# Optimization experiments

Hardware: AMD Instinct MI355X
Metric: run time of the kernel (lower is better)

The kernel has to match this reference:

```python
import math
import jax, jax.numpy as jnp
from jax import lax
import numpy as np

SQRT2 = 1.4142135623730951
LR_MLP = 0.01


def _blur_kernel():
    k = jnp.array([1., 3., 3., 1.], dtype=jnp.float32)
    k = k[:, None] * k[None, :]
    return k / jnp.sum(k)


def upfirdn2d(x, kernel, up, pad0, pad1):
    # x: (B,C,H,W). Matches torch upfirdn2d_native (flip kernel, zero-upsample, pad, correlate).
    B, C, H, W = x.shape
    x = x.reshape(B * C, 1, H, W)
    k = jnp.flip(kernel, (0, 1))[None, None]
    p1 = pad1 + (up - 1)  # lax lhs_dilation omits trailing zeros of upfirdn upsampling
    out = lax.conv_general_dilated(x, k, (1, 1), ((pad0, p1), (pad0, p1)), lhs_dilation=(up, up))
    return out.reshape(B, C, out.shape[-2], out.shape[-1])


def pixel_norm(x, eps=1e-6):
    norm = jnp.sqrt(jnp.sum(x * x, axis=1, keepdims=True))
    norm = norm / math.sqrt(x.shape[1])
    return x / (norm + eps)


def fused_act(x, b):
    return jax.nn.leaky_relu(x + b[None, :, None, None], 0.2) * SQRT2


def mod_conv(x, w, sw, sb, lat, demodulate, up):
    # w: (Cout,Cin,kh,kw); sw: (Cin, style_ch) equalized-lr linear; lat: (B, style_ch)
    Cout, Cin, kh, kw = w.shape
    s = lat @ (sw.T * (1.0 / math.sqrt(sw.shape[1]))) + sb  # (B, Cin), bias_init=1
    wm = (w * (1.0 / math.sqrt(Cin * kh * kw)))[None] * s[:, None, :, None, None]
    if demodulate:
        d = lax.rsqrt(jnp.sum(wm * wm, axis=(2, 3, 4)) + 1e-8)
        wm = wm * d[:, :, None, None, None]
    if up:
        # per-sample conv_transpose(stride=2, pad=0) == dilated conv with flipped kernel
        def f(xi, wi):
            return lax.conv_general_dilated(xi[None], jnp.flip(wi, (2, 3)), (1, 1),
                                            ((kh - 1, kh - 1), (kw - 1, kw - 1)),
                                            lhs_dilation=(2, 2))[0]
        out = jax.vmap(f)(x, wm)
        out = upfirdn2d(out, _blur_kernel() * 4.0, 1, 1, 1)  # Blur pad=(1,1), k*factor^2
    else:
        pad = kh // 2
        def f(xi, wi):
            return lax.conv_general_dilated(xi[None], wi, (1, 1), ((pad, pad), (pad, pad)))[0]
        out = jax.vmap(f)(x, wm)
    return out


def style_mapping(z, W, Bv):
    x = pixel_norm(z)
    sc = 1.0 / math.sqrt(W.shape[-1])
    for i in range(W.shape[0]):
        x = jax.nn.leaky_relu(x @ (W[i].T * sc) + Bv[i] * LR_MLP, 0.2) * SQRT2
    return x


def setup_inputs() -> dict:
    key = jax.random.key(0)
    ks = jax.random.split(key, 32)
    B = 32
    inp = {
        'z': jax.random.normal(ks[0], (B, 512), jnp.float32),
        'mlp_w': jax.random.normal(ks[1], (8, 512, 512), jnp.float32),
        'mlp_b': jax.random.normal(ks[2], (8, 512), jnp.float32),
        'const_input': jax.random.normal(ks[3], (1, 512, 4, 4), jnp.float32),
        'conv_w': jax.random.normal(ks[4], (9, 512, 512, 3, 3), jnp.float32),
        'conv_style_w': jax.random.normal(ks[5], (9, 512, 512), jnp.float32),
        'conv_style_b': jnp.ones((9, 512), jnp.float32),
        'noise_w': jax.random.normal(ks[6], (9,), jnp.float32),
        'act_bias': jnp.zeros((9, 512), jnp.float32),
        'torgb_w': jax.random.normal(ks[7], (5, 3, 512, 1, 1), jnp.float32),
        'torgb_style_w': jax.random.normal(ks[8], (5, 512, 512), jnp.float32),
        'torgb_style_b': jnp.ones((5, 512), jnp.float32),
        'torgb_bias': jnp.zeros((5, 3), jnp.float32),
    }
    sizes = [4, 8, 8, 16, 16, 32, 32, 64, 64]
    for i, s in enumerate(sizes):
        inp[f'noise{i}'] = jax.random.normal(ks[10 + i], (B, 1, s, s), jnp.float32)
    return inp


def reference(z, mlp_w, mlp_b, const_input, conv_w, conv_style_w, conv_style_b,
              noise_w, act_bias, torgb_w, torgb_style_w, torgb_style_b, torgb_bias,
              noise0, noise1, noise2, noise3, noise4, noise5, noise6, noise7, noise8):
    noises = [noise0, noise1, noise2, noise3, noise4, noise5, noise6, noise7, noise8]
    w = style_mapping(z, mlp_w, mlp_b)  # single style injection -> same w for all layers
    B = z.shape[0]
    x = jnp.tile(const_input, (B, 1, 1, 1))

    def sconv(x, i, up):
        out = mod_conv(x, conv_w[i], conv_style_w[i], conv_style_b[i], w, True, up)
        out = out + noise_w[i] * noises[i]
        return fused_act(out, act_bias[i])

    def trgb(x, j):
        out = mod_conv(x, torgb_w[j], torgb_style_w[j], torgb_style_b[j], w, False, False)
        return out + torgb_bias[j][None, :, None, None]

    x = sconv(x, 0, False)
    skip = trgb(x, 0)
    bk = _blur_kernel() * 4.0
    for r in range(4):  # resolutions 8,16,32,64
        x = sconv(x, 1 + 2 * r, True)
        x = sconv(x, 2 + 2 * r, False)
        skip = trgb(x, r + 1) + upfirdn2d(skip, bk, 2, 2, 1)  # UpsampleUpFIRDn pad=(2,1)
    return skip  # (B,3,64,64)
```

## Files before the change

kernel.cpp:

```cpp
#include <hip/hip_runtime.h>
#include <hip/hip_bf16.h>
#include <cstdio>
#include <math.h>


static constexpr int NB = 32;
static constexpr float SQRT2F      = 1.41421356237309515f;
static constexpr float INV_SQRT512 = 0.04419417382415922f;
static constexpr float INV_SQRT4608= 0.014731391274719742f;

typedef __hip_bfloat16 bf16;
typedef __attribute__((ext_vector_type(8))) short bf16x8;
typedef __attribute__((ext_vector_type(4))) float f32x4;

__device__ __forceinline__ float lrelu_s2(float v){ return (v > 0.f ? v : 0.2f*v) * SQRT2F; }
__device__ __forceinline__ float bf_lo(unsigned u){ unsigned v = u << 16; return __builtin_bit_cast(float, v); }
__device__ __forceinline__ float bf_hi(unsigned u){ unsigned v = u & 0xffff0000u; return __builtin_bit_cast(float, v); }
__device__ __forceinline__ unsigned packbf2(float a, float b){
  bf16 ha = __float2bfloat16(a), hb = __float2bfloat16(b);
  unsigned short ra = __builtin_bit_cast(unsigned short, ha);
  unsigned short rb = __builtin_bit_cast(unsigned short, hb);
  return (unsigned)ra | ((unsigned)rb << 16);
}

__global__ void k_mapping(const float* __restrict__ z, const float* __restrict__ mlp_w,
                          const float* __restrict__ mlp_b, float* __restrict__ wlat){
  __shared__ float xb[512], yb[512], red[256];
  int b = blockIdx.x, t = threadIdx.x;
  float z0 = z[b*512 + t], z1 = z[b*512 + t + 256];
  red[t] = z0*z0 + z1*z1;
  __syncthreads();
  for(int s = 128; s > 0; s >>= 1){ if(t < s) red[t] += red[t+s]; __syncthreads(); }
  float norm = sqrtf(red[0]) * INV_SQRT512;
  float inv = 1.f / (norm + 1e-6f);
  xb[t] = z0*inv; xb[t+256] = z1*inv;
  __syncthreads();
  for(int l = 0; l < 8; l++){
    const float* Wl = mlp_w + (size_t)l*512*512;
    const float* bl = mlp_b + l*512;
    for(int oo = 0; oo < 2; oo++){
      int o = t + oo*256;
      const float4* wr = (const float4*)(Wl + (size_t)o*512);
      float acc = 0.f;
      #pragma unroll 4
      for(int k = 0; k < 128; k++){
        float4 w4 = wr[k];
        acc += w4.x*xb[4*k] + w4.y*xb[4*k+1] + w4.z*xb[4*k+2] + w4.w*xb[4*k+3];
      }
      yb[o] = lrelu_s2(acc*INV_SQRT512 + bl[o]*0.01f);
    }
    __syncthreads();
    xb[t] = yb[t]; xb[t+256] = yb[t+256];
    __syncthreads();
  }
  wlat[b*512+t] = xb[t]; wlat[b*512+t+256] = xb[t+256];
}

__global__ void k_styles(const float* __restrict__ wlat,
                         const float* __restrict__ csw, const float* __restrict__ csb,
                         const float* __restrict__ tsw, const float* __restrict__ tsb,
                         float* __restrict__ s_conv, float* __restrict__ s_trgb){
  int gid = blockIdx.x*256 + threadIdx.x;
  int l = gid >> 14;
  int b = (gid >> 9) & 31;
  int i = gid & 511;
  const float* row; float bias, wsc;
  if(l < 9){ row = csw + ((size_t)l*512 + i)*512; bias = csb[l*512+i]; wsc = INV_SQRT4608; }
  else     { int lt = l-9; row = tsw + ((size_t)lt*512 + i)*512; bias = tsb[lt*512+i]; wsc = INV_SQRT512; }
  const float4* r4 = (const float4*)row;
  const float4* w4 = (const float4*)(wlat + b*512);
  float acc = 0.f;
  #pragma unroll 4
  for(int k = 0; k < 128; k++){
    float4 a = w4[k], c = r4[k];
    acc += a.x*c.x + a.y*c.y + a.z*c.z + a.w*c.w;
  }
  float s = (acc*INV_SQRT512 + bias) * wsc;
  if(l < 9) s_conv[((size_t)l*32 + b)*512 + i] = s;
  else      s_trgb[((size_t)(l-9)*32 + b)*512 + i] = s;
}

__global__ void k_wsq(const float* __restrict__ cw, float* __restrict__ wsq){
  int gid = blockIdx.x*256 + threadIdx.x;
  const float* p = cw + (size_t)gid*9;
  float a = 0.f;
  #pragma unroll
  for(int t = 0; t < 9; t++){ float v = p[t]; a += v*v; }
  wsq[gid] = a;
}

__global__ void k_demod(const float* __restrict__ s_conv, const float* __restrict__ wsq,
                        float* __restrict__ d_conv){
  __shared__ float s2[512];
  int l = blockIdx.x/32, b = blockIdx.x%32, t = threadIdx.x;
  size_t base = ((size_t)l*32 + b)*512;
  float v0 = s_conv[base + t], v1 = s_conv[base + t + 256];
  s2[t] = v0*v0; s2[t+256] = v1*v1;
  __syncthreads();
  for(int oo = 0; oo < 2; oo++){
    int o = t + oo*256;
    const float4* wr = (const float4*)(wsq + ((size_t)l*512 + o)*512);
    float acc = 0.f;
    #pragma unroll 4
    for(int k = 0; k < 128; k++){
      float4 w = wr[k];
      acc += w.x*s2[4*k] + w.y*s2[4*k+1] + w.z*s2[4*k+2] + w.w*s2[4*k+3];
    }
    d_conv[base + o] = rsqrtf(acc + 1e-8f);
  }
}

__global__ void k_ratio(const float* __restrict__ s_conv, const float* __restrict__ s_trgb,
                        float* __restrict__ rat){
  int gid = blockIdx.x*256 + threadIdx.x;
  int lt = gid >> 14;
  if(lt >= 4){ rat[gid] = 1.0f; return; }
  int b = (gid >> 9) & 31;
  int i = gid & 511;
  int cl = 1 + 2*lt;
  float st = s_trgb[((size_t)lt*32 + b)*512 + i];
  float sc = s_conv[((size_t)cl*32 + b)*512 + i];
  rat[gid] = (sc != 0.f) ? st/sc : 0.f;
}

__global__ void k_wB(const float* __restrict__ cw, bf16* __restrict__ wB){
  int gid = blockIdx.x*256 + threadIdx.x;
  const float* p = cw + (size_t)gid*9;
  int l = gid >> 18;
  int oi = gid & 0x3ffff;
  #pragma unroll
  for(int tap = 0; tap < 9; tap++)
    wB[((size_t)(l*9 + tap) << 18) + oi] = __float2bfloat16(p[tap]);
}

__global__ void k_init(const float* __restrict__ ci, const float* __restrict__ s_conv,
                       bf16* __restrict__ act){
  int gid = blockIdx.x*256 + threadIdx.x;
  int c = gid & 511; int px = (gid >> 9) & 15; int b = gid >> 13;
  act[gid] = __float2bfloat16(ci[c*16 + px] * s_conv[b*512 + c]);
}

template<bool UP>
__global__ __launch_bounds__(256, 2)
void k_conv(const bf16* __restrict__ act, const bf16* __restrict__ wL,
            const float* __restrict__ dL, const float* __restrict__ noise,
            const float* __restrict__ nw_ptr, const float* __restrict__ ab,
            const float* __restrict__ sN, bf16* __restrict__ outp,
            int Hin, int Mblocks){
  const int q8 = gridDim.x >> 3;
  const int swz = (blockIdx.x & 7)*q8 + (blockIdx.x >> 3);
  const int nb = swz & 3, mb = swz >> 2;
  if(mb >= Mblocks) return;
  const int mbase = mb*128, nbase = nb*128;

  int py = 0, px = 0;
  int OHy, OHx;
  if(UP){
    int cls = blockIdx.z; py = cls >> 1; px = cls & 1;
    OHy = Hin + 1 - py; OHx = Hin + 1 - px;
  } else {
    OHy = Hin; OHx = Hin;
  }
  const int pixN = OHy*OHx;
  const int Mtot = NB*pixN;
  if(mbase >= Mtot) return;

  __shared__ short As[2][128*40];
  __shared__ short Bs[2][128*40];
  const int t = threadIdx.x;
  const int slot = t & 3;
  const int rowq[2] = {t >> 2, (t >> 2) + 64};

  int gb[2], gY[2], gX[2]; bool mval[2];
  #pragma unroll
  for(int q = 0; q < 2; q++){
    int m = mbase + rowq[q];
    mval[q] = (m < Mtot);
    int mm = mval[q] ? m : 0;
    gb[q] = mm / pixN; int rem = mm % pixN; gY[q] = rem / OHx; gX[q] = rem % OHx;
  }

  const int wid = t >> 6;
  const int mrow0 = (wid >> 1)*64;
  const int ncol0 = (wid & 1)*64;
  const int lr = t & 15;
  const int ks = (t & 63) >> 4;

  f32x4 acc[4][4];
  #pragma unroll
  for(int i = 0; i < 4; i++)
    #pragma unroll
    for(int j = 0; j < 4; j++) acc[i][j] = (f32x4){0.f,0.f,0.f,0.f};

  int dyl[3], dxl[3], ndy, ndx;
  if(UP){
    if(py == 0){ dyl[0]=0; dyl[1]=2; ndy=2; } else { dyl[0]=1; ndy=1; }
    if(px == 0){ dxl[0]=0; dxl[1]=2; ndx=2; } else { dxl[0]=1; ndx=1; }
  } else {
    dyl[0]=0; dyl[1]=1; dyl[2]=2; ndy=3;
    dxl[0]=0; dxl[1]=1; dxl[2]=2; ndx=3;
  }
  const int TT = ndy*ndx;

  for(int tt = 0; tt < TT; tt++){
    const int dy = dyl[tt/ndx], dx = dxl[tt%ndx];
    const int tap = dy*3 + dx;
    const bf16* aptr[2]; bool aok[2];
    #pragma unroll
    for(int q = 0; q < 2; q++){
      aok[q] = false; aptr[q] = act;
      if(mval[q]){
        int yy, xx;
        if(UP){ yy = gY[q] - ((dy - py) >> 1); xx = gX[q] - ((dx - px) >> 1); }
        else  { yy = gY[q] + dy - 1;           xx = gX[q] + dx - 1; }
        if((unsigned)yy < (unsigned)Hin && (unsigned)xx < (unsigned)Hin){
          aok[q] = true;
          aptr[q] = act + ((size_t)((gb[q]*Hin + yy)*Hin + xx) << 9) + slot*8;
        }
      }
    }
    const bf16* bptr[2];
    #pragma unroll
    for(int q = 0; q < 2; q++)
      bptr[q] = wL + (((size_t)tap*512 + nbase + rowq[q]) << 9) + slot*8;

    uint4 pa[2][2], pb[2][2];
    #pragma unroll
    for(int q = 0; q < 2; q++)
      #pragma unroll
      for(int h = 0; h < 2; h++){
        pa[q][h] = aok[q] ? *(const uint4*)(aptr[q] + h*32) : make_uint4(0u,0u,0u,0u);
        pb[q][h] = *(const uint4*)(bptr[q] + h*32);
      }

    #pragma unroll
    for(int c = 0; c < 8; c++){
      asm volatile("" ::: "memory");
      __builtin_amdgcn_s_barrier();
      #pragma unroll
      for(int q = 0; q < 2; q++)
        #pragma unroll
        for(int h = 0; h < 2; h++){
          *(uint4*)&As[h][rowq[q]*40 + slot*8] = pa[q][h];
          *(uint4*)&Bs[h][rowq[q]*40 + slot*8] = pb[q][h];
        }
      uint4 na[2][2], nb4[2][2];
      if(c < 7){
        const int koff = (c+1)*64;
        #pragma unroll
        for(int q = 0; q < 2; q++)
          #pragma unroll
          for(int h = 0; h < 2; h++){
            na[q][h]  = aok[q] ? *(const uint4*)(aptr[q] + koff + h*32) : make_uint4(0u,0u,0u,0u);
            nb4[q][h] = *(const uint4*)(bptr[q] + koff + h*32);
          }
      }
      asm volatile("s_waitcnt lgkmcnt(0)" ::: "memory");
      __builtin_amdgcn_s_barrier();
      #pragma unroll
      for(int h = 0; h < 2; h++){
        bf16x8 af[4], bfr[4];
        #pragma unroll
        for(int f = 0; f < 4; f++){
          af[f]  = *(const bf16x8*)&As[h][(mrow0 + f*16 + lr)*40 + ks*8];
          bfr[f] = *(const bf16x8*)&Bs[h][(ncol0 + f*16 + lr)*40 + ks*8];
        }
        #pragma unroll
        for(int mf = 0; mf < 4; mf++)
          #pragma unroll
          for(int nf = 0; nf < 4; nf++)
            acc[mf][nf] = __builtin_amdgcn_mfma_f32_16x16x32_bf16(af[mf], bfr[nf], acc[mf][nf], 0, 0, 0);
      }
      if(c < 7){
        #pragma unroll
        for(int q = 0; q < 2; q++)
          #pragma unroll
          for(int h = 0; h < 2; h++){ pa[q][h] = na[q][h]; pb[q][h] = nb4[q][h]; }
      }
    }
  }

  const float nwv = UP ? 0.f : *nw_ptr;
  const int U = 2*Hin + 1;
  #pragma unroll
  for(int mf = 0; mf < 4; mf++){
    #pragma unroll
    for(int r = 0; r < 4; r++){
      int m = mbase + mrow0 + mf*16 + ks*4 + r;
      if(m >= Mtot) continue;
      int b = m / pixN; int rem = m % pixN; int y = rem / OHx, x = rem % OHx;
      const float* drow = dL + b*512;
      bf16* orow;
      float nz = 0.f; const float* srow = nullptr;
      if(UP){
        orow = outp + (((size_t)((b*U + 2*y + py))*U + (2*x + px)) << 9);
      } else {
        nz = nwv * noise[(b*OHy + y)*OHx + x];
        srow = sN + b*512;
        orow = outp + ((size_t)m << 9);
      }
      #pragma unroll
      for(int nf = 0; nf < 4; nf++){
        int n = nbase + ncol0 + nf*16 + lr;
        float val = acc[mf][nf][r] * drow[n];
        if(!UP) val = lrelu_s2(val + nz + ab[n]) * srow[n];
        orow[n] = __float2bfloat16(val);
      }
    }
  }
}

__global__ void k_blur(const bf16* __restrict__ u, const float* __restrict__ noise,
                       const float* __restrict__ nw_ptr, const float* __restrict__ ab,
                       const float* __restrict__ sN, bf16* __restrict__ act, int O){
  const int U = O + 1;
  size_t gid = (size_t)blockIdx.x*256 + threadIdx.x;
  size_t total = (size_t)NB*O*O*128;
  if(gid >= total) return;
  int c4 = gid & 127;
  size_t pix = gid >> 7;
  int X = pix % O; int Y = (pix/O) % O; int b = pix/((size_t)O*O);
  const float k1[4] = {1.f, 3.f, 3.f, 1.f};
  float4 a = make_float4(0.f,0.f,0.f,0.f);
  #pragma unroll
  for(int ky = 0; ky < 4; ky++){
    int yy = Y + ky - 1; if(yy < 0 || yy >= U) continue;
    #pragma unroll
    for(int kx = 0; kx < 4; kx++){
      int xx = X + kx - 1; if(xx < 0 || xx >= U) continue;
      float w = k1[ky]*k1[kx]*(1.f/16.f);
      uint2 u2 = *(const uint2*)(u + (((size_t)(b*U + yy)*U + xx) << 9) + c4*4);
      a.x += w*bf_lo(u2.x); a.y += w*bf_hi(u2.x);
      a.z += w*bf_lo(u2.y); a.w += w*bf_hi(u2.y);
    }
  }
  float nz = (*nw_ptr) * noise[(b*O + Y)*O + X];
  const float* abp4 = ab + c4*4;
  float4 s4 = *(const float4*)(sN + b*512 + c4*4);
  uint2 pk;
  pk.x = packbf2(lrelu_s2(a.x + nz + abp4[0])*s4.x, lrelu_s2(a.y + nz + abp4[1])*s4.y);
  pk.y = packbf2(lrelu_s2(a.z + nz + abp4[2])*s4.z, lrelu_s2(a.w + nz + abp4[3])*s4.w);
  *(uint2*)(act + (pix << 9) + c4*4) = pk;
}

__global__ void k_torgb(const bf16* __restrict__ act, const float* __restrict__ tw,
                        const float* __restrict__ ratL, const float* __restrict__ tbias,
                        float* __restrict__ dst, int H, int lt, int addflag){
  int wid = threadIdx.x >> 6, lane = threadIdx.x & 63;
  int pix = blockIdx.x*4 + wid;
  int npix = NB*H*H;
  if(pix >= npix) return;
  int b = pix/(H*H);
  const bf16* ap = act + ((size_t)pix << 9);
  const float* rp = ratL + (size_t)b*512;
  const float* w0 = tw + ((size_t)lt*3 + 0)*512;
  const float* w1 = tw + ((size_t)lt*3 + 1)*512;
  const float* w2 = tw + ((size_t)lt*3 + 2)*512;
  float a0 = 0.f, a1 = 0.f, a2 = 0.f;
  #pragma unroll
  for(int j = 0; j < 8; j++){
    int i = lane + j*64;
    float xs = __bfloat162float(ap[i])*rp[i];
    a0 += xs*w0[i]; a1 += xs*w1[i]; a2 += xs*w2[i];
  }
  for(int off = 32; off > 0; off >>= 1){
    a0 += __shfl_xor(a0, off);
    a1 += __shfl_xor(a1, off);
    a2 += __shfl_xor(a2, off);
  }
  if(lane == 0){
    int rem = pix % (H*H);
    size_t o0 = ((size_t)(b*3 + 0)*H*H) + rem;
    size_t o1 = ((size_t)(b*3 + 1)*H*H) + rem;
    size_t o2 = ((size_t)(b*3 + 2)*H*H) + rem;
    float b0 = tbias[lt*3+0], b1 = tbias[lt*3+1], b2 = tbias[lt*3+2];
    if(addflag){ dst[o0] += a0 + b0; dst[o1] += a1 + b1; dst[o2] += a2 + b2; }
    else       { dst[o0]  = a0 + b0; dst[o1]  = a1 + b1; dst[o2]  = a2 + b2; }
  }
}

__global__ void k_skipup(const float* __restrict__ sin, float* __restrict__ sout, int h){
  const int O = 2*h;
  int gid = blockIdx.x*256 + threadIdx.x;
  int total = NB*3*O*O;
  if(gid >= total) return;
  int X = gid % O; int Y = (gid/O) % O; int c = (gid/(O*O)) % 3; int b = gid/(3*O*O);
  const float k1[4] = {1.f, 3.f, 3.f, 1.f};
  float acc = 0.f;
  for(int ky = (Y & 1); ky < 4; ky += 2){
    int ty = Y + ky - 2;
    if(ty < 0) continue;
    int y = ty >> 1; if(y >= h) continue;
    for(int kx = (X & 1); kx < 4; kx += 2){
      int tx = X + kx - 2;
      if(tx < 0) continue;
      int x = tx >> 1; if(x >= h) continue;
      acc += k1[ky]*k1[kx]*(1.f/16.f) * sin[((size_t)(b*3 + c)*h + y)*h + x];
    }
  }
  sout[gid] = acc;
}

extern "C" void kernel_launch(void* const* d_in, const int* in_sizes, int n_in,
                              void* d_out, int out_size, void* d_ws, size_t ws_size,
                              hipStream_t stream){
  const float* z     = (const float*)d_in[0];
  const float* mlp_w = (const float*)d_in[1];
  const float* mlp_b = (const float*)d_in[2];
  const float* cinp  = (const float*)d_in[3];
  const float* conv_w= (const float*)d_in[4];
  const float* csw   = (const float*)d_in[5];
  const float* csb   = (const float*)d_in[6];
  const float* nwp   = (const float*)d_in[7];
  const float* abp   = (const float*)d_in[8];
  const float* tw    = (const float*)d_in[9];
  const float* tsw   = (const float*)d_in[10];
  const float* tsb   = (const float*)d_in[11];
  const float* tb    = (const float*)d_in[12];
  const float* noise[9];
  for(int i = 0; i < 9; i++) noise[i] = (const float*)d_in[13 + i];

  const size_t UMAX = (size_t)32*65*65*512;
  char* base = (char*)d_ws;
  size_t off = 0;
  bf16* buf0 = (bf16*)(base + off); off += UMAX*2;
  bf16* buf1 = (bf16*)(base + off); off += UMAX*2;
  bf16* wB   = (bf16*)(base + off); off += (size_t)9*9*512*512*2;
  float* wsq = (float*)(base + off); off += (size_t)9*512*512*4;
  float* wlat= (float*)(base + off); off += (size_t)32*512*4;
  float* sconv=(float*)(base + off); off += (size_t)9*32*512*4;
  float* dconv=(float*)(base + off); off += (size_t)9*32*512*4;
  float* strgb=(float*)(base + off); off += (size_t)5*32*512*4;
  float* rat  =(float*)(base + off); off += (size_t)5*32*512*4;
  float* skipA=(float*)(base + off); off += (size_t)32*3*64*64*4;
  float* skipB=(float*)(base + off); off += (size_t)32*3*64*64*4;
  if(ws_size < off){
    fprintf(stderr, "kernel_launch: ws too small (%zu < %zu)\n", ws_size, off);
    return;
  }
  float* out = (float*)d_out;

  k_mapping<<<32, 256, 0, stream>>>(z, mlp_w, mlp_b, wlat);
  k_styles <<<896, 256, 0, stream>>>(wlat, csw, csb, tsw, tsb, sconv, strgb);
  k_wsq    <<<9216, 256, 0, stream>>>(conv_w, wsq);
  k_demod  <<<288, 256, 0, stream>>>(sconv, wsq, dconv);
  k_ratio  <<<320, 256, 0, stream>>>(sconv, strgb, rat);
  k_wB     <<<9216, 256, 0, stream>>>(conv_w, wB);
  k_init   <<<1024, 256, 0, stream>>>(cinp, sconv, buf0);

  auto conv_noup = [&](const bf16* in, bf16* o, int H, int layer, const float* sN){
    int M = 32*H*H; int Mb = (M + 127)/128;
    int Gx = ((Mb*4 + 7)/8)*8;
    k_conv<false><<<dim3(Gx,1,1), 256, 0, stream>>>(in, wB + ((size_t)layer*9 << 18),
        dconv + (size_t)layer*NB*512, noise[layer], nwp + layer, abp + layer*512, sN, o, H, Mb);
  };
  auto conv_up = [&](const bf16* in, bf16* o, int Hin, int layer){
    int Mmax = 32*(Hin+1)*(Hin+1); int Mb = (Mmax + 127)/128;
    int Gx = ((Mb*4 + 7)/8)*8;
    k_conv<true><<<dim3(Gx,1,4), 256, 0, stream>>>(in, wB + ((size_t)layer*9 << 18),
        dconv + (size_t)layer*NB*512, nullptr, nullptr, nullptr, nullptr, o, Hin, Mb);
  };
  auto blur = [&](const bf16* u, bf16* o, int O, int layer, const float* sN){
    size_t total = (size_t)32*O*O*128;
    k_blur<<<(unsigned)((total + 255)/256), 256, 0, stream>>>(u, noise[layer], nwp + layer,
        abp + layer*512, sN, o, O);
  };
  auto torgb = [&](const bf16* act, float* dst, int H, int lt, int add){
    int npix = 32*H*H;
    k_torgb<<<(npix + 3)/4, 256, 0, stream>>>(act, tw, rat + (size_t)lt*NB*512, tb, dst, H, lt, add);
  };
  auto skipup = [&](const float* sin, float* sout, int h){
    int total = 32*3*(2*h)*(2*h);
    k_skipup<<<(total + 255)/256, 256, 0, stream>>>(sin, sout, h);
  };

  const float* S = sconv;
  const float* sT4 = strgb + (size_t)4*NB*512;

  conv_noup(buf0, buf1, 4, 0, S + (size_t)1*NB*512);
  torgb(buf1, skipA, 4, 0, 0);

  conv_up(buf1, buf0, 4, 1);
  blur(buf0, buf1, 8, 1, S + (size_t)2*NB*512);
  conv_noup(buf1, buf0, 8, 2, S + (size_t)3*NB*512);
  skipup(skipA, skipB, 4);
  torgb(buf0, skipB, 8, 1, 1);

  conv_up(buf0, buf1, 8, 3);
  blur(buf1, buf0, 16, 3, S + (size_t)4*NB*512);
  conv_noup(buf0, buf1, 16, 4, S + (size_t)5*NB*512);
  skipup(skipB, skipA, 8);
  torgb(buf1, skipA, 16, 2, 1);

  conv_up(buf1, buf0, 16, 5);
  blur(buf0, buf1, 32, 5, S + (size_t)6*NB*512);
  conv_noup(buf1, buf0, 32, 6, S + (size_t)7*NB*512);
  skipup(skipA, skipB, 16);
  torgb(buf0, skipB, 32, 3, 1);

  conv_up(buf0, buf1, 32, 7);
  blur(buf1, buf0, 64, 7, S + (size_t)8*NB*512);
  conv_noup(buf0, buf1, 64, 8, sT4);
  skipup(skipB, out, 32);
  torgb(buf1, out, 64, 4, 1);
}
```

Measured before the change: 2.528 ms.

## Fuse weight prep kernels and flatten conv tap/K loop into single pipelined loop

Merges the weight-squared and bf16 weight-transpose kernels into one pass over conv weights, so the fp32 weights are read once instead of twice. In the conv kernel, the per-tap outer loop plus unrolled 8-chunk inner loop become a single flattened loop over tap×chunk. The next tap's first chunk is now prefetched during the current tap's last compute, which removes the pipeline bubble at each tap boundary. Each thread now loads one row with two 16-element halves instead of two rows, which changes the global load pattern and adds per-iteration tap-setup logic.

```diff
diff --git a/kernel.cpp b/kernel.cpp
--- a/kernel.cpp
+++ b/kernel.cpp
@@ -80,13 +80,19 @@
   else      s_trgb[((size_t)(l-9)*32 + b)*512 + i] = s;
 }
 
-__global__ void k_wsq(const float* __restrict__ cw, float* __restrict__ wsq){
+__global__ void k_prep(const float* __restrict__ cw, float* __restrict__ wsq,
+                       bf16* __restrict__ wB){
   int gid = blockIdx.x*256 + threadIdx.x;
   const float* p = cw + (size_t)gid*9;
-  float a = 0.f;
-  #pragma unroll
-  for(int t = 0; t < 9; t++){ float v = p[t]; a += v*v; }
+  int l = gid >> 18;
+  int oi = gid & 0x3ffff;
+  float v[9]; float a = 0.f;
+  #pragma unroll
+  for(int t = 0; t < 9; t++){ v[t] = p[t]; a += v[t]*v[t]; }
   wsq[gid] = a;
+  #pragma unroll
+  for(int tap = 0; tap < 9; tap++)
+    wB[((size_t)(l*9 + tap) << 18) + oi] = __float2bfloat16(v[tap]);
 }
 
 __global__ void k_demod(const float* __restrict__ s_conv, const float* __restrict__ wsq,
@@ -123,16 +129,6 @@
   rat[gid] = (sc != 0.f) ? st/sc : 0.f;
 }
 
-__global__ void k_wB(const float* __restrict__ cw, bf16* __restrict__ wB){
-  int gid = blockIdx.x*256 + threadIdx.x;
-  const float* p = cw + (size_t)gid*9;
-  int l = gid >> 18;
-  int oi = gid & 0x3ffff;
-  #pragma unroll
-  for(int tap = 0; tap < 9; tap++)
-    wB[((size_t)(l*9 + tap) << 18) + oi] = __float2bfloat16(p[tap]);
-}
-
 __global__ void k_init(const float* __restrict__ ci, const float* __restrict__ s_conv,
                        bf16* __restrict__ act){
   int gid = blockIdx.x*256 + threadIdx.x;
@@ -168,17 +164,14 @@
   __shared__ short As[2][128*40];
   __shared__ short Bs[2][128*40];
   const int t = threadIdx.x;
-  const int slot = t & 3;
-  const int rowq[2] = {t >> 2, (t >> 2) + 64};
-
-  int gb[2], gY[2], gX[2]; bool mval[2];
-  #pragma unroll
-  for(int q = 0; q < 2; q++){
-    int m = mbase + rowq[q];
-    mval[q] = (m < Mtot);
-    int mm = mval[q] ? m : 0;
-    gb[q] = mm / pixN; int rem = mm % pixN; gY[q] = rem / OHx; gX[q] = rem % OHx;
-  }
+  const int row = t & 127;
+  const int sp  = (t >> 7) & 1;
+
+  int m = mbase + row;
+  const bool mval = (m < Mtot);
+  int mm = mval ? m : 0;
+  const int gb = mm / pixN; int rem = mm % pixN;
+  const int gY = rem / OHx, gX = rem % OHx;
 
   const int wid = t >> 6;
   const int mrow0 = (wid >> 1)*64;
@@ -192,91 +185,84 @@
     #pragma unroll
     for(int j = 0; j < 4; j++) acc[i][j] = (f32x4){0.f,0.f,0.f,0.f};
 
-  int dyl[3], dxl[3], ndy, ndx;
-  if(UP){
-    if(py == 0){ dyl[0]=0; dyl[1]=2; ndy=2; } else { dyl[0]=1; ndy=1; }
-    if(px == 0){ dxl[0]=0; dxl[1]=2; ndx=2; } else { dxl[0]=1; ndx=1; }
-  } else {
-    dyl[0]=0; dyl[1]=1; dyl[2]=2; ndy=3;
-    dxl[0]=0; dxl[1]=1; dxl[2]=2; ndx=3;
-  }
+  int ndy, ndx;
+  if(UP){ ndy = (py==0)?2:1; ndx = (px==0)?2:1; } else { ndy = 3; ndx = 3; }
   const int TT = ndy*ndx;
-
-  for(int tt = 0; tt < TT; tt++){
-    const int dy = dyl[tt/ndx], dx = dxl[tt%ndx];
-    const int tap = dy*3 + dx;
-    const bf16* aptr[2]; bool aok[2];
-    #pragma unroll
-    for(int q = 0; q < 2; q++){
-      aok[q] = false; aptr[q] = act;
-      if(mval[q]){
-        int yy, xx;
-        if(UP){ yy = gY[q] - ((dy - py) >> 1); xx = gX[q] - ((dx - px) >> 1); }
-        else  { yy = gY[q] + dy - 1;           xx = gX[q] + dx - 1; }
-        if((unsigned)yy < (unsigned)Hin && (unsigned)xx < (unsigned)Hin){
-          aok[q] = true;
-          aptr[q] = act + ((size_t)((gb[q]*Hin + yy)*Hin + xx) << 9) + slot*8;
+  const int TOT = TT*8;
+
+  const bf16* browB = wL + (((size_t)(nbase + row)) << 9) + sp*16;
+
+  const bf16* aptr = act; const bf16* bptr = browB; bool aok = false;
+  auto setTap = [&](int tt){
+    int iy, ix;
+    if(!UP){ iy = (tt*11) >> 5; ix = tt - iy*3; }
+    else   { iy = (ndx==2) ? (tt>>1) : tt; ix = tt & (ndx-1); }
+    int dy = UP ? ((py==0) ? iy*2 : 1) : iy;
+    int dx = UP ? ((px==0) ? ix*2 : 1) : ix;
+    int yy, xx;
+    if(UP){ yy = gY - ((dy - py) >> 1); xx = gX - ((dx - px) >> 1); }
+    else  { yy = gY + dy - 1;           xx = gX + dx - 1; }
+    aok = mval && ((unsigned)yy < (unsigned)Hin) && ((unsigned)xx < (unsigned)Hin);
+    aptr = act + ((size_t)((gb*Hin + yy)*Hin + xx) << 9) + sp*16;
+    bptr = browB + ((size_t)(dy*3 + dx) << 18);
+  };
+
+  setTap(0);
+  uint4 pa[2][2], pb[2][2];
+  #pragma unroll
+  for(int h = 0; h < 2; h++)
+    #pragma unroll
+    for(int j = 0; j < 2; j++){
+      pa[h][j] = aok ? *(const uint4*)(aptr + h*32 + j*8) : make_uint4(0u,0u,0u,0u);
+      pb[h][j] = *(const uint4*)(bptr + h*32 + j*8);
+    }
+
+  for(int it = 0; it < TOT; ++it){
+    asm volatile("" ::: "memory");
+    __builtin_amdgcn_s_barrier();
+    #pragma unroll
+    for(int h = 0; h < 2; h++)
+      #pragma unroll
+      for(int j = 0; j < 2; j++){
+        *(uint4*)&As[h][row*40 + sp*16 + j*8] = pa[h][j];
+        *(uint4*)&Bs[h][row*40 + sp*16 + j*8] = pb[h][j];
+      }
+    uint4 na[2][2], nb4[2][2];
+    const bool have = (it + 1 < TOT);
+    if(have){
+      const int itn = it + 1;
+      const int cn = itn & 7;
+      if(cn == 0) setTap(itn >> 3);
+      const int icc = cn*64;
+      #pragma unroll
+      for(int h = 0; h < 2; h++)
+        #pragma unroll
+        for(int j = 0; j < 2; j++){
+          na[h][j]  = aok ? *(const uint4*)(aptr + icc + h*32 + j*8) : make_uint4(0u,0u,0u,0u);
+          nb4[h][j] = *(const uint4*)(bptr + icc + h*32 + j*8);
         }
+    }
+    asm volatile("s_waitcnt lgkmcnt(0)" ::: "memory");
+    __builtin_amdgcn_s_barrier();
+    #pragma unroll
+    for(int h = 0; h < 2; h++){
+      bf16x8 af[4], bfr[4];
+      #pragma unroll
+      for(int f = 0; f < 4; f++){
+        af[f]  = *(const bf16x8*)&As[h][(mrow0 + f*16 + lr)*40 + ks*8];
+        bfr[f] = *(const bf16x8*)&Bs[h][(ncol0 + f*16 + lr)*40 + ks*8];
       }
-    }
-    const bf16* bptr[2];
-    #pragma unroll
-    for(int q = 0; q < 2; q++)
-      bptr[q] = wL + (((size_t)tap*512 + nbase + rowq[q]) << 9) + slot*8;
-
-    uint4 pa[2][2], pb[2][2];
-    #pragma unroll
-    for(int q = 0; q < 2; q++)
-      #pragma unroll
-      for(int h = 0; h < 2; h++){
-        pa[q][h] = aok[q] ? *(const uint4*)(aptr[q] + h*32) : make_uint4(0u,0u,0u,0u);
-        pb[q][h] = *(const uint4*)(bptr[q] + h*32);
-      }
-
-    #pragma unroll
-    for(int c = 0; c < 8; c++){
-      asm volatile("" ::: "memory");
-      __builtin_amdgcn_s_barrier();
-      #pragma unroll
-      for(int q = 0; q < 2; q++)
+      #pragma unroll
+      for(int mf = 0; mf < 4; mf++)
         #pragma unroll
-        for(int h = 0; h < 2; h++){
-          *(uint4*)&As[h][rowq[q]*40 + slot*8] = pa[q][h];
-          *(uint4*)&Bs[h][rowq[q]*40 + slot*8] = pb[q][h];
-        }
-      uint4 na[2][2], nb4[2][2];
-      if(c < 7){
-        const int koff = (c+1)*64;
+        for(int nf = 0; nf < 4; nf++)
+          acc[mf][nf] = __builtin_amdgcn_mfma_f32_16x16x32_bf16(af[mf], bfr[nf], acc[mf][nf], 0, 0, 0);
+    }
+    if(have){
+      #pragma unroll
+      for(int h = 0; h < 2; h++)
         #pragma unroll
-        for(int q = 0; q < 2; q++)
-          #pragma unroll
-          for(int h = 0; h < 2; h++){
-            na[q][h]  = aok[q] ? *(const uint4*)(aptr[q] + koff + h*32) : make_uint4(0u,0u,0u,0u);
-            nb4[q][h] = *(const uint4*)(bptr[q] + koff + h*32);
-          }
-      }
-      asm volatile("s_waitcnt lgkmcnt(0)" ::: "memory");
-      __builtin_amdgcn_s_barrier();
-      #pragma unroll
-      for(int h = 0; h < 2; h++){
-        bf16x8 af[4], bfr[4];
-        #pragma unroll
-        for(int f = 0; f < 4; f++){
-          af[f]  = *(const bf16x8*)&As[h][(mrow0 + f*16 + lr)*40 + ks*8];
-          bfr[f] = *(const bf16x8*)&Bs[h][(ncol0 + f*16 + lr)*40 + ks*8];
-        }
-        #pragma unroll
-        for(int mf = 0; mf < 4; mf++)
-          #pragma unroll
-          for(int nf = 0; nf < 4; nf++)
-            acc[mf][nf] = __builtin_amdgcn_mfma_f32_16x16x32_bf16(af[mf], bfr[nf], acc[mf][nf], 0, 0, 0);
-      }
-      if(c < 7){
-        #pragma unroll
-        for(int q = 0; q < 2; q++)
-          #pragma unroll
-          for(int h = 0; h < 2; h++){ pa[q][h] = na[q][h]; pb[q][h] = nb4[q][h]; }
-      }
+        for(int j = 0; j < 2; j++){ pa[h][j] = na[h][j]; pb[h][j] = nb4[h][j]; }
     }
   }
 
@@ -286,9 +272,9 @@
   for(int mf = 0; mf < 4; mf++){
     #pragma unroll
     for(int r = 0; r < 4; r++){
-      int m = mbase + mrow0 + mf*16 + ks*4 + r;
-      if(m >= Mtot) continue;
-      int b = m / pixN; int rem = m % pixN; int y = rem / OHx, x = rem % OHx;
+      int me = mbase + mrow0 + mf*16 + ks*4 + r;
+      if(me >= Mtot) continue;
+      int b = me / pixN; int rem2 = me % pixN; int y = rem2 / OHx, x = rem2 % OHx;
       const float* drow = dL + b*512;
       bf16* orow;
       float nz = 0.f; const float* srow = nullptr;
@@ -297,7 +283,7 @@
       } else {
         nz = nwv * noise[(b*OHy + y)*OHx + x];
         srow = sN + b*512;
-        orow = outp + ((size_t)m << 9);
+        orow = outp + ((size_t)me << 9);
       }
       #pragma unroll
       for(int nf = 0; nf < 4; nf++){
@@ -442,10 +428,9 @@
 
   k_mapping<<<32, 256, 0, stream>>>(z, mlp_w, mlp_b, wlat);
   k_styles <<<896, 256, 0, stream>>>(wlat, csw, csb, tsw, tsb, sconv, strgb);
-  k_wsq    <<<9216, 256, 0, stream>>>(conv_w, wsq);
+  k_prep   <<<9216, 256, 0, stream>>>(conv_w, wsq, wB);
   k_demod  <<<288, 256, 0, stream>>>(sconv, wsq, dconv);
   k_ratio  <<<320, 256, 0, stream>>>(sconv, strgb, rat);
-  k_wB     <<<9216, 256, 0, stream>>>(conv_w, wB);
   k_init   <<<1024, 256, 0, stream>>>(cinp, sconv, buf0);
 
   auto conv_noup = [&](const bf16* in, bf16* o, int H, int layer, const float* sN){
```

After: 7.554 ms. 199% more time.
